# Kernel optimization log

Measured on AMD Instinct MI355X. Metric: run time of the kernel, lower is better.

Reference implementation:

```python
import jax, jax.numpy as jnp
import numpy as np

USER_NUM, ITEM_NUM = 50000, 25000
N_U, N_I = 4096, 4096
N_E, N_PRED = 262144, 65536
D, K, N_LAYERS = 64, 1000, 3
SSL_TEMP, SSL_REG, ALPHA, PROTO_REG = 0.1, 1e-6, 1.0, 8e-8


def setup_inputs() -> dict:
    key = jax.random.key(0)
    ks = jax.random.split(key, 16)
    return {
        "emb_user": jax.random.normal(ks[0], (USER_NUM, D), jnp.float32),
        "emb_item": jax.random.normal(ks[1], (ITEM_NUM, D), jnp.float32),
        "user_centroids": jax.random.normal(ks[2], (K, D), jnp.float32),
        "item_centroids": jax.random.normal(ks[3], (K, D), jnp.float32),
        "edge_u": jax.random.randint(ks[4], (N_E,), 0, N_U, jnp.int32),
        "edge_v": jax.random.randint(ks[5], (N_E,), 0, N_I, jnp.int32),
        "pos_u": jax.random.randint(ks[6], (N_PRED,), 0, N_U, jnp.int32),
        "pos_v": jax.random.randint(ks[7], (N_PRED,), 0, N_I, jnp.int32),
        "neg_u": jax.random.randint(ks[8], (N_PRED,), 0, N_U, jnp.int32),
        "neg_v": jax.random.randint(ks[9], (N_PRED,), 0, N_I, jnp.int32),
        "idx_user": jax.random.randint(ks[10], (N_U,), 0, USER_NUM, jnp.int32),
        "idx_item": jax.random.randint(ks[11], (N_I,), 0, ITEM_NUM, jnp.int32),
        "user2cluster": jax.random.randint(ks[12], (USER_NUM,), 0, K, jnp.int32),
        "item2cluster": jax.random.randint(ks[13], (ITEM_NUM,), 0, K, jnp.int32),
    }


def _l2norm(x, eps=1e-12):  # F.normalize(p=2, dim=1)
    return x / jnp.maximum(jnp.linalg.norm(x, axis=1, keepdims=True), eps)


def _ssl_loss(cur, prev, prev_total):
    nc, npv, nt = _l2norm(cur), _l2norm(prev), _l2norm(prev_total)
    pos = jnp.exp(jnp.sum(nc * npv, axis=1) / SSL_TEMP)            # [B]
    tot = jnp.exp(nc @ nt.T / SSL_TEMP).sum(axis=1)                 # [B]
    return -jnp.log(pos / tot).sum()


def _proto_loss(emb, idx, node2cluster, centroids):
    ne = _l2norm(emb)
    cents = _l2norm(centroids)                                      # run_kmeans normalizes centroids
    my_cent = cents[node2cluster[idx]]                              # [B, D]
    pos = jnp.exp(jnp.sum(ne * my_cent, axis=1) / SSL_TEMP)
    tot = jnp.exp(ne @ cents.T / SSL_TEMP).sum(axis=1)
    return -jnp.log(pos / tot).sum()


def reference(emb_user, emb_item, user_centroids, item_centroids,
              edge_u, edge_v, pos_u, pos_v, neg_u, neg_v,
              idx_user, idx_item, user2cluster, item2cluster):
    # --- symmetric-normalized bipartite GraphConv (norm='both', no weight/bias) ---
    ones_e = jnp.ones((N_E,), jnp.float32)
    deg_u = jax.ops.segment_sum(ones_e, edge_u, num_segments=N_U)
    deg_i = jax.ops.segment_sum(ones_e, edge_v, num_segments=N_I)
    inv_u = (1.0 / jnp.sqrt(jnp.maximum(deg_u, 1.0)))[:, None]      # [N_U,1]
    inv_i = (1.0 / jnp.sqrt(jnp.maximum(deg_i, 1.0)))[:, None]      # [N_I,1]

    e_u = emb_user[idx_user]                                        # initial subgraph embeddings
    e_i = emb_item[idx_item]
    res_u, res_i = e_u, e_i
    h_u, h_i = e_u, e_i
    for _ in range(N_LAYERS):
        m_u = (h_u * inv_u)[edge_u]                                 # messages along rate edges
        m_i = (h_i * inv_i)[edge_v]                                 # messages along rated-by edges
        new_i = jax.ops.segment_sum(m_u, edge_v, num_segments=N_I) * inv_i
        new_u = jax.ops.segment_sum(m_i, edge_u, num_segments=N_U) * inv_u
        h_u, h_i = new_u, new_i
        res_u = res_u + h_u
        res_i = res_i + h_i

    # --- structural-neighbour SSL loss (last layer output vs layer-0 embeddings) ---
    ssl_u = _ssl_loss(h_u, e_u, emb_user)
    ssl_i = _ssl_loss(h_i, e_i, emb_item)
    ssl_loss = SSL_REG * (ssl_u + ALPHA * ssl_i)

    # --- protoNCE loss (raw embedding-table rows vs kmeans centroids) ---
    proto_loss = PROTO_REG * (
        _proto_loss(emb_user[idx_user], idx_user, user2cluster, user_centroids)
        + _proto_loss(emb_item[idx_item], idx_item, item2cluster, item_centroids)
    )

    res_u = res_u / (N_LAYERS + 1)
    res_i = res_i / (N_LAYERS + 1)

    # --- HeteroDotProductPredictor: u_dot_v on 'rate' edges -> [E,1] ---
    pos_score = jnp.sum(res_u[pos_u] * res_i[pos_v], axis=1, keepdims=True)
    neg_score = jnp.sum(res_u[neg_u] * res_i[neg_v], axis=1, keepdims=True)
    return pos_score, neg_score, ssl_loss, proto_loss
```

## Files before the change

kernel.cpp:

```cpp
#include <hip/hip_runtime.h>
#include <hip/hip_bf16.h>

#define NU 4096
#define NI 4096
#define NE 262144
#define NPRED 65536
#define DD 64
#define KCL 1000
#define UNUM 50000
#define INUM 25000
#define INUM_PAD 25008
#define KCL_PAD 1008

typedef short sh8 __attribute__((ext_vector_type(8)));
typedef float f4 __attribute__((ext_vector_type(4)));

__device__ __forceinline__ float wred64(float x){
#pragma unroll
  for(int m=1;m<64;m<<=1) x += __shfl_xor(x,m);
  return x;
}

__device__ __forceinline__ float fast_exp2(float x){
  return __builtin_amdgcn_exp2f(x);
}

__global__ void k_hist(const int* __restrict__ eu, const int* __restrict__ ev,
                       int* cu, int* ci){
  int t = blockIdx.x*256 + threadIdx.x;
  if(t < NE){ atomicAdd(&cu[eu[t]],1); atomicAdd(&ci[ev[t]],1); }
}

__global__ void k_scan(const int* cnt_u, int* rp_u, int* cur_u, float* inv_u,
                       const int* cnt_i, int* rp_i, int* cur_i, float* inv_i){
  const int* cnt = blockIdx.x ? cnt_i : cnt_u;
  int* rp  = blockIdx.x ? rp_i  : rp_u;
  int* cur = blockIdx.x ? cur_i : cur_u;
  float* inv = blockIdx.x ? inv_i : inv_u;
  __shared__ int sdata[1024];
  int tid = threadIdx.x;
  int v[4]; int s = 0;
#pragma unroll
  for(int k=0;k<4;k++){ v[k]=cnt[tid*4+k]; s+=v[k]; }
  sdata[tid]=s; __syncthreads();
  for(int off=1; off<1024; off<<=1){
    int add = (tid>=off)? sdata[tid-off] : 0;
    __syncthreads();
    if(tid>=off) sdata[tid] += add;
    __syncthreads();
  }
  int run = sdata[tid]-s;
#pragma unroll
  for(int k=0;k<4;k++){
    int idx = tid*4+k;
    rp[idx]=run; cur[idx]=run;
    inv[idx] = 1.0f/sqrtf(fmaxf((float)v[k],1.0f));
    run += v[k];
  }
  if(tid==1023) rp[4096]=run;
}

__global__ void k_fill(const int* __restrict__ eu, const int* __restrict__ ev,
                       int* cur_u, int* cur_i, int* adj_u, int* adj_i){
  int t = blockIdx.x*256 + threadIdx.x;
  if(t < NE){
    int u=eu[t], v=ev[t];
    adj_u[atomicAdd(&cur_u[u],1)] = v;
    adj_i[atomicAdd(&cur_i[v],1)] = u;
  }
}

__global__ void k_gather(const float* __restrict__ emb_u, const float* __restrict__ emb_i,
                         const int* __restrict__ idx_u, const int* __restrict__ idx_i,
                         const float* __restrict__ inv_u, const float* __restrict__ inv_i,
                         float* e_u, float* e_i, float* res_u, float* res_i,
                         float* hs_u, float* hs_i){
  int t = blockIdx.x*256 + threadIdx.x;
  const int half = NU*DD;
  if(t < half){
    int r=t>>6;
    float v = emb_u[idx_u[r]*DD + (t&63)];
    e_u[t]=v; res_u[t]=v; hs_u[t]=v*inv_u[r];
  } else {
    int s=t-half; int r=s>>6;
    float v = emb_i[idx_i[r]*DD + (s&63)];
    e_i[s]=v; res_i[s]=v; hs_i[s]=v*inv_i[r];
  }
}

__global__ void k_conv(const int* __restrict__ rp_i, const int* __restrict__ adj_i,
                       const float* __restrict__ hsu_in, const float* __restrict__ inv_i,
                       float* h_i, float* res_i, float* hsi_out,
                       const int* __restrict__ rp_u, const int* __restrict__ adj_u,
                       const float* __restrict__ hsi_in, const float* __restrict__ inv_u,
                       float* h_u, float* res_u, float* hsu_out){
  int b = blockIdx.x, lane = threadIdx.x;
  const int* rp; const int* adj; const float* srcv; const float* inv;
  float *h, *res, *hso; int node;
  if(b < NI){ rp=rp_i; adj=adj_i; srcv=hsu_in; inv=inv_i; h=h_i; res=res_i; hso=hsi_out; node=b; }
  else      { node=b-NI; rp=rp_u; adj=adj_u; srcv=hsi_in; inv=inv_u; h=h_u; res=res_u; hso=hsu_out; }
  int s=rp[node], e=rp[node+1];
  float acc=0.f;
  for(int base=s; base<e; base+=64){
    int m = e-base;
    int myidx = adj[base + min(lane, m-1)];
    int kk = min(64, m);
    int k=0;
    for(; k+8<=kk; k+=8){
      int i0=__shfl(myidx,k  ), i1=__shfl(myidx,k+1),
          i2=__shfl(myidx,k+2), i3=__shfl(myidx,k+3),
          i4=__shfl(myidx,k+4), i5=__shfl(myidx,k+5),
          i6=__shfl(myidx,k+6), i7=__shfl(myidx,k+7);
      float v0=srcv[i0*DD+lane], v1=srcv[i1*DD+lane],
            v2=srcv[i2*DD+lane], v3=srcv[i3*DD+lane],
            v4=srcv[i4*DD+lane], v5=srcv[i5*DD+lane],
            v6=srcv[i6*DD+lane], v7=srcv[i7*DD+lane];
      acc += ((v0+v1)+(v2+v3)) + ((v4+v5)+(v6+v7));
    }
    for(; k<kk; k++) acc += srcv[__shfl(myidx,k)*DD+lane];
  }
  float iv = inv[node];
  float outv = acc*iv;
  h[node*DD+lane] = outv;
  res[node*DD+lane] += outv;
  hso[node*DD+lane] = outv*iv;
}

#define SB0 12500
#define SB1 (SB0+6252)
#define SB2 (SB1+252)
#define SB3 (SB2+252)
#define SB4 (SB3+1024)
#define SB5 (SB4+1024)
#define SB6 (SB5+1024)
#define SB7 (SB6+1024)

__global__ void k_normall(const float* __restrict__ emb_u, const float* __restrict__ emb_i,
                          const float* __restrict__ ucent, const float* __restrict__ icent,
                          const float* __restrict__ h_u, const float* __restrict__ h_i,
                          const float* __restrict__ e_u, const float* __restrict__ e_i,
                          __hip_bfloat16* ntb_u, __hip_bfloat16* ntb_i,
                          __hip_bfloat16* ncb_u, __hip_bfloat16* ncb_i,
                          __hip_bfloat16* nc_u, __hip_bfloat16* nc_i,
                          __hip_bfloat16* npv_u, __hip_bfloat16* npv_i){
  const float SC = 14.426950408889634f;
  int b = blockIdx.x;
  const float* in; __hip_bfloat16* outp; int rows; float scale; int base;
  if(b < SB0)      { in=emb_u; outp=ntb_u; rows=UNUM; scale=1.f;  base=0; }
  else if(b < SB1) { in=emb_i; outp=ntb_i; rows=INUM; scale=1.f;  base=SB0; }
  else if(b < SB2) { in=ucent; outp=ncb_u; rows=KCL;  scale=1.f;  base=SB1; }
  else if(b < SB3) { in=icent; outp=ncb_i; rows=KCL;  scale=1.f;  base=SB2; }
  else if(b < SB4) { in=h_u;   outp=nc_u;  rows=NU;   scale=SC;   base=SB3; }
  else if(b < SB5) { in=h_i;   outp=nc_i;  rows=NI;   scale=SC;   base=SB4; }
  else if(b < SB6) { in=e_u;   outp=npv_u; rows=NU;   scale=SC;   base=SB5; }
  else             { in=e_i;   outp=npv_i; rows=NI;   scale=SC;   base=SB6; }
  int row = (b-base)*4 + (threadIdx.x>>6);
  int lane = threadIdx.x & 63;
  if(row >= rows){
    outp[row*DD + lane] = __float2bfloat16(0.f);
    return;
  }
  float v = in[row*DD + lane];
  float s = wred64(v*v);
  float sc = scale / fmaxf(sqrtf(s), 1e-12f);
  outp[row*DD + lane] = __float2bfloat16(v*sc);
}

__global__ void k_pos(const float* __restrict__ h_u, const float* __restrict__ h_i,
                      const float* __restrict__ e_u, const float* __restrict__ e_i,
                      const float* __restrict__ cent_u, const float* __restrict__ cent_i,
                      const int* __restrict__ idx_u, const int* __restrict__ idx_i,
                      const int* __restrict__ u2c, const int* __restrict__ i2c,
                      float* pos4){
  int w = blockIdx.x*4 + (threadIdx.x>>6);
  int lane = threadIdx.x & 63;
  if(w >= NU) return;
  float hu=h_u[w*DD+lane], eu=e_u[w*DD+lane];
  float hi=h_i[w*DD+lane], ei=e_i[w*DD+lane];
  int cu = u2c[idx_u[w]], ci = i2c[idx_i[w]];
  float cuv = cent_u[cu*DD+lane], civ = cent_i[ci*DD+lane];
  float hh = wred64(hu*hu), ee = wred64(eu*eu), he = wred64(hu*eu);
  float h2 = wred64(hi*hi), e2 = wred64(ei*ei), hei= wred64(hi*ei);
  float ccu= wred64(cuv*cuv), ecu = wred64(eu*cuv);
  float cci= wred64(civ*civ), eci = wred64(ei*civ);
  if(lane==0){
    const float eps=1e-12f;
    pos4[0*NU+w] = he  / (fmaxf(sqrtf(hh),eps)*fmaxf(sqrtf(ee),eps));
    pos4[1*NU+w] = hei / (fmaxf(sqrtf(h2),eps)*fmaxf(sqrtf(e2),eps));
    pos4[2*NU+w] = ecu / (fmaxf(sqrtf(ee),eps)*fmaxf(sqrtf(ccu),eps));
    pos4[3*NU+w] = eci / (fmaxf(sqrtf(e2),eps)*fmaxf(sqrtf(cci),eps));
  }
}

struct EArg {
  const __hip_bfloat16* A; const __hip_bfloat16* B; float* tot;
  int nBpad; int jchunk; int ny;
};

__global__ __launch_bounds__(256,4)
void k_expsum(EArg e0, EArg e1, EArg e2, EArg e3){
  EArg e = (blockIdx.z==0)? e0 : (blockIdx.z==1)? e1 : (blockIdx.z==2)? e2 : e3;
  int bid = blockIdx.x;
  int g = bid >> 6, r6 = bid & 63;
  int y = 8*g + (r6 & 7);
  int x = r6 >> 3;
  if(y >= e.ny) return;
  int wave = threadIdx.x >> 6;
  int lane = threadIdx.x & 63;
  int row0 = (x*4 + wave)*128;
  int j_begin = y*e.jchunk;
  int j_end = min(j_begin + e.jchunk, e.nBpad);
  int r = lane & 15, kq = (lane>>4)*8;

  sh8 a0[8], a1[8];
#pragma unroll
  for(int t=0;t<8;t++){
    const short* ap = (const short*)(e.A + (row0 + t*16 + r)*DD);
    a0[t] = *(const sh8*)(ap + kq);
    a1[t] = *(const sh8*)(ap + kq + 32);
  }
  float acc[8][4];
#pragma unroll
  for(int t=0;t<8;t++)
#pragma unroll
    for(int q=0;q<4;q++) acc[t][q]=0.f;

  const short* bbase = (const short*)e.B;
  const short* bp0 = bbase + (j_begin + r)*DD + kq;
  sh8 b0 = *(const sh8*)(bp0);
  sh8 b1 = *(const sh8*)(bp0 + 32);

#pragma unroll 2
  for(int j0=j_begin; j0<j_end; j0+=16){
    const short* np = bbase + (j0 + 16 + r)*DD + kq;
    sh8 n0 = *(const sh8*)(np);
    sh8 n1 = *(const sh8*)(np + 32);
#pragma unroll
    for(int t=0;t<8;t++){
      f4 c = {0.f,0.f,0.f,0.f};
      c = __builtin_amdgcn_mfma_f32_16x16x32_bf16(a0[t], b0, c, 0,0,0);
      c = __builtin_amdgcn_mfma_f32_16x16x32_bf16(a1[t], b1, c, 0,0,0);
#pragma unroll
      for(int q=0;q<4;q++) acc[t][q] += fast_exp2(c[q]);
    }
    b0 = n0; b1 = n1;
  }
#pragma unroll
  for(int t=0;t<8;t++){
#pragma unroll
    for(int q=0;q<4;q++){
      float v = acc[t][q];
      v += __shfl_xor(v,1); v += __shfl_xor(v,2);
      v += __shfl_xor(v,4); v += __shfl_xor(v,8);
      if(r==0) atomicAdd(&e.tot[row0 + t*16 + (lane>>4)*4 + q], v);
    }
  }
}

__global__ void k_score(const float* __restrict__ res_u, const float* __restrict__ res_i,
                        const int* __restrict__ pu, const int* __restrict__ pv,
                        const int* __restrict__ nu, const int* __restrict__ nv,
                        float* out){
  int t = blockIdx.x*256 + threadIdx.x;
  int pair = t >> 4;
  int sl = t & 15;
  if(pair >= 2*NPRED) return;
  int a,b;
  if(pair < NPRED){ a=pu[pair]; b=pv[pair]; }
  else { a=nu[pair-NPRED]; b=nv[pair-NPRED]; }
  f4 xu = *(const f4*)(res_u + a*DD + sl*4);
  f4 xv = *(const f4*)(res_i + b*DD + sl*4);
  float x = xu[0]*xv[0] + xu[1]*xv[1] + xu[2]*xv[2] + xu[3]*xv[3];
  x += __shfl_xor(x,1); x += __shfl_xor(x,2);
  x += __shfl_xor(x,4); x += __shfl_xor(x,8);
  if(sl==0) out[pair] = x*(1.0f/16.0f);
}

__global__ void k_loss(const float* __restrict__ tot4, const float* __restrict__ pos4,
                       float* out){
  const float PI_ = (float)(INUM_PAD-INUM), PK_ = (float)(KCL_PAD-KCL);
  float s0=0,s1=0,s2=0,s3=0;
  for(int b=threadIdx.x; b<NU; b+=256){
    s0 += logf(tot4[0*NU+b])       - 10.f*pos4[0*NU+b];
    s1 += logf(tot4[1*NU+b] - PI_) - 10.f*pos4[1*NU+b];
    s2 += logf(tot4[2*NU+b] - PK_) - 10.f*pos4[2*NU+b];
    s3 += logf(tot4[3*NU+b] - PK_) - 10.f*pos4[3*NU+b];
  }
  s0=wred64(s0); s1=wred64(s1); s2=wred64(s2); s3=wred64(s3);
  __shared__ float ls[4][4];
  int lane=threadIdx.x&63, w=threadIdx.x>>6;
  if(lane==0){ ls[w][0]=s0; ls[w][1]=s1; ls[w][2]=s2; ls[w][3]=s3; }
  __syncthreads();
  if(threadIdx.x==0){
    float a=0,b2=0,c=0,d=0;
#pragma unroll
    for(int k=0;k<4;k++){ a+=ls[k][0]; b2+=ls[k][1]; c+=ls[k][2]; d+=ls[k][3]; }
    out[2*NPRED]   = 1e-6f*(a+b2);
    out[2*NPRED+1] = 8e-8f*(c+d);
  }
}

extern "C" void kernel_launch(void* const* d_in, const int* in_sizes, int n_in,
                              void* d_out, int out_size, void* d_ws, size_t ws_size,
                              hipStream_t stream) {
  const float* emb_user = (const float*)d_in[0];
  const float* emb_item = (const float*)d_in[1];
  const float* ucent    = (const float*)d_in[2];
  const float* icent    = (const float*)d_in[3];
  const int* edge_u = (const int*)d_in[4];
  const int* edge_v = (const int*)d_in[5];
  const int* pos_u  = (const int*)d_in[6];
  const int* pos_v  = (const int*)d_in[7];
  const int* neg_u  = (const int*)d_in[8];
  const int* neg_v  = (const int*)d_in[9];
  const int* idx_u  = (const int*)d_in[10];
  const int* idx_i  = (const int*)d_in[11];
  const int* u2c    = (const int*)d_in[12];
  const int* i2c    = (const int*)d_in[13];
  float* out = (float*)d_out;

  char* w = (char*)d_ws;
  auto alloc = [&](size_t bytes)->void*{
    void* p = (void*)w;
    w += (bytes + 255) & ~(size_t)255;
    return p;
  };
  int* cnt_u = (int*)alloc(NU*4);
  int* cnt_i = (int*)alloc(NI*4);
  int* rp_u  = (int*)alloc((NU+1)*4);
  int* rp_i  = (int*)alloc((NI+1)*4);
  int* cur_u = (int*)alloc(NU*4);
  int* cur_i = (int*)alloc(NI*4);
  int* adj_u = (int*)alloc((size_t)NE*4);
  int* adj_i = (int*)alloc((size_t)NE*4);
  float* inv_u = (float*)alloc(NU*4);
  float* inv_i = (float*)alloc(NI*4);
  float* e_u  = (float*)alloc((size_t)NU*DD*4);
  float* e_i  = (float*)alloc((size_t)NI*DD*4);
  float* h_u  = (float*)alloc((size_t)NU*DD*4);
  float* h_i  = (float*)alloc((size_t)NI*DD*4);
  float* hsA_u = (float*)alloc((size_t)NU*DD*4);
  float* hsA_i = (float*)alloc((size_t)NI*DD*4);
  float* hsB_u = (float*)alloc((size_t)NU*DD*4);
  float* hsB_i = (float*)alloc((size_t)NI*DD*4);
  float* res_u= (float*)alloc((size_t)NU*DD*4);
  float* res_i= (float*)alloc((size_t)NI*DD*4);
  __hip_bfloat16* ntb_user = (__hip_bfloat16*)alloc((size_t)(UNUM+48)*DD*2);
  __hip_bfloat16* ntb_item = (__hip_bfloat16*)alloc((size_t)(INUM_PAD+48)*DD*2);
  __hip_bfloat16* ncb_u = (__hip_bfloat16*)alloc((size_t)(KCL_PAD+48)*DD*2);
  __hip_bfloat16* ncb_i = (__hip_bfloat16*)alloc((size_t)(KCL_PAD+48)*DD*2);
  __hip_bfloat16* nc_u  = (__hip_bfloat16*)alloc((size_t)NU*DD*2);
  __hip_bfloat16* nc_i  = (__hip_bfloat16*)alloc((size_t)NI*DD*2);
  __hip_bfloat16* npv_u = (__hip_bfloat16*)alloc((size_t)NU*DD*2);
  __hip_bfloat16* npv_i = (__hip_bfloat16*)alloc((size_t)NI*DD*2);
  float* tot4 = (float*)alloc(4*NU*4);
  float* pos4 = (float*)alloc(4*NU*4);

  hipMemsetAsync(cnt_u, 0, NU*4, stream);
  hipMemsetAsync(cnt_i, 0, NI*4, stream);
  hipMemsetAsync(tot4, 0, 4*NU*4, stream);

  k_hist<<<NE/256, 256, 0, stream>>>(edge_u, edge_v, cnt_u, cnt_i);
  k_scan<<<2, 1024, 0, stream>>>(cnt_u, rp_u, cur_u, inv_u, cnt_i, rp_i, cur_i, inv_i);
  k_fill<<<NE/256, 256, 0, stream>>>(edge_u, edge_v, cur_u, cur_i, adj_u, adj_i);
  k_gather<<<2*NU*DD/256, 256, 0, stream>>>(emb_user, emb_item, idx_u, idx_i,
                                            inv_u, inv_i,
                                            e_u, e_i, res_u, res_i, hsA_u, hsA_i);
  k_conv<<<NU+NI, 64, 0, stream>>>(rp_i, adj_i, hsA_u, inv_i, h_i, res_i, hsB_i,
                                   rp_u, adj_u, hsA_i, inv_u, h_u, res_u, hsB_u);
  k_conv<<<NU+NI, 64, 0, stream>>>(rp_i, adj_i, hsB_u, inv_i, h_i, res_i, hsA_i,
                                   rp_u, adj_u, hsB_i, inv_u, h_u, res_u, hsA_u);
  k_conv<<<NU+NI, 64, 0, stream>>>(rp_i, adj_i, hsA_u, inv_i, h_i, res_i, hsB_i,
                                   rp_u, adj_u, hsA_i, inv_u, h_u, res_u, hsB_u);

  k_normall<<<SB7, 256, 0, stream>>>(emb_user, emb_item, ucent, icent,
                                     h_u, h_i, e_u, e_i,
                                     ntb_user, ntb_item, ncb_u, ncb_i,
                                     nc_u, nc_i, npv_u, npv_i);

  k_pos<<<NU/4, 256, 0, stream>>>(h_u, h_i, e_u, e_i, ucent, icent,
                                  idx_u, idx_i, u2c, i2c, pos4);

  EArg eu_ = { nc_u,  ntb_user, tot4 + 0*NU, UNUM,     1024, 49 };
  EArg ei_ = { nc_i,  ntb_item, tot4 + 1*NU, INUM_PAD, 1024, 25 };
  EArg ep0 = { npv_u, ncb_u,    tot4 + 2*NU, KCL_PAD,  48,   21 };
  EArg ep1 = { npv_i, ncb_i,    tot4 + 3*NU, KCL_PAD,  48,   21 };
  k_expsum<<<dim3(448,1,4), 256, 0, stream>>>(eu_, ei_, ep0, ep1);

  k_score<<<(2*NPRED*16)/256, 256, 0, stream>>>(res_u, res_i, pos_u, pos_v, neg_u, neg_v, out);
  k_loss<<<1, 256, 0, stream>>>(tot4, pos4, out);
}
```

Before: 239.1 us.

## Rebalance expsum work into uniform chunks with persistent grid; pack conv waves per block

The exp-sum GEMM kernel now uses a flat work list of fixed 256-column chunks across all four segments, processed by a persistent 1024-block grid with a grid-stride loop. This replaces the old 3D grid with uneven per-segment chunk sizes and many early-exit blocks, aiming for better load balance across CUs. The conv kernel packs four node-waves into each 256-thread block instead of one wave per block, which cuts block scheduling overhead. Smaller chunks mean more atomicAdds per output row and more reloads of the A fragments.

```diff
diff --git a/kernel.cpp b/kernel.cpp
--- a/kernel.cpp
+++ b/kernel.cpp
@@ -94,7 +94,8 @@
                        const int* __restrict__ rp_u, const int* __restrict__ adj_u,
                        const float* __restrict__ hsi_in, const float* __restrict__ inv_u,
                        float* h_u, float* res_u, float* hsu_out){
-  int b = blockIdx.x, lane = threadIdx.x;
+  int b = blockIdx.x*4 + (threadIdx.x>>6);
+  int lane = threadIdx.x & 63;
   const int* rp; const int* adj; const float* srcv; const float* inv;
   float *h, *res, *hso; int node;
   if(b < NI){ rp=rp_i; adj=adj_i; srcv=hsu_in; inv=inv_i; h=h_i; res=res_i; hso=hsi_out; node=b; }
@@ -192,67 +193,73 @@
   }
 }
 
-struct EArg {
-  const __hip_bfloat16* A; const __hip_bfloat16* B; float* tot;
-  int nBpad; int jchunk; int ny;
-};
+#define ECH 256
+#define EU0 1568
+#define EU1 (EU0+784)
+#define EU2 (EU1+32)
+#define EU3 (EU2+32)
+
+struct ESeg { const __hip_bfloat16* A; const __hip_bfloat16* B; float* tot; int nB; };
 
 __global__ __launch_bounds__(256,4)
-void k_expsum(EArg e0, EArg e1, EArg e2, EArg e3){
-  EArg e = (blockIdx.z==0)? e0 : (blockIdx.z==1)? e1 : (blockIdx.z==2)? e2 : e3;
-  int bid = blockIdx.x;
-  int g = bid >> 6, r6 = bid & 63;
-  int y = 8*g + (r6 & 7);
-  int x = r6 >> 3;
-  if(y >= e.ny) return;
+void k_expsum(ESeg s0, ESeg s1, ESeg s2, ESeg s3){
   int wave = threadIdx.x >> 6;
   int lane = threadIdx.x & 63;
-  int row0 = (x*4 + wave)*128;
-  int j_begin = y*e.jchunk;
-  int j_end = min(j_begin + e.jchunk, e.nBpad);
   int r = lane & 15, kq = (lane>>4)*8;
 
-  sh8 a0[8], a1[8];
-#pragma unroll
-  for(int t=0;t<8;t++){
-    const short* ap = (const short*)(e.A + (row0 + t*16 + r)*DD);
-    a0[t] = *(const sh8*)(ap + kq);
-    a1[t] = *(const sh8*)(ap + kq + 32);
-  }
-  float acc[8][4];
-#pragma unroll
-  for(int t=0;t<8;t++)
-#pragma unroll
-    for(int q=0;q<4;q++) acc[t][q]=0.f;
-
-  const short* bbase = (const short*)e.B;
-  const short* bp0 = bbase + (j_begin + r)*DD + kq;
-  sh8 b0 = *(const sh8*)(bp0);
-  sh8 b1 = *(const sh8*)(bp0 + 32);
+  for(int u = blockIdx.x; u < EU3; u += 1024){
+    ESeg s; int rem;
+    if(u < EU0)      { s = s0; rem = u; }
+    else if(u < EU1) { s = s1; rem = u-EU0; }
+    else if(u < EU2) { s = s2; rem = u-EU1; }
+    else             { s = s3; rem = u-EU2; }
+    int yc = rem >> 3, x = rem & 7;
+    int row0 = (x*4 + wave)*128;
+    int j_begin = yc*ECH;
+    int j_end = min(j_begin + ECH, s.nB);
+
+    sh8 a0[8], a1[8];
+#pragma unroll
+    for(int t=0;t<8;t++){
+      const short* ap = (const short*)(s.A + (row0 + t*16 + r)*DD);
+      a0[t] = *(const sh8*)(ap + kq);
+      a1[t] = *(const sh8*)(ap + kq + 32);
+    }
+    float acc[8][4];
+#pragma unroll
+    for(int t=0;t<8;t++)
+#pragma unroll
+      for(int q=0;q<4;q++) acc[t][q]=0.f;
+
+    const short* bbase = (const short*)s.B;
+    const short* bp0 = bbase + (j_begin + r)*DD + kq;
+    sh8 b0 = *(const sh8*)(bp0);
+    sh8 b1 = *(const sh8*)(bp0 + 32);
 
 #pragma unroll 2
-  for(int j0=j_begin; j0<j_end; j0+=16){
-    const short* np = bbase + (j0 + 16 + r)*DD + kq;
-    sh8 n0 = *(const sh8*)(np);
-    sh8 n1 = *(const sh8*)(np + 32);
+    for(int j0=j_begin; j0<j_end; j0+=16){
+      const short* np = bbase + (j0 + 16 + r)*DD + kq;
+      sh8 n0 = *(const sh8*)(np);
+      sh8 n1 = *(const sh8*)(np + 32);
+#pragma unroll
+      for(int t=0;t<8;t++){
+        f4 c = {0.f,0.f,0.f,0.f};
+        c = __builtin_amdgcn_mfma_f32_16x16x32_bf16(a0[t], b0, c, 0,0,0);
+        c = __builtin_amdgcn_mfma_f32_16x16x32_bf16(a1[t], b1, c, 0,0,0);
+#pragma unroll
+        for(int q=0;q<4;q++) acc[t][q] += fast_exp2(c[q]);
+      }
+      b0 = n0; b1 = n1;
+    }
 #pragma unroll
     for(int t=0;t<8;t++){
-      f4 c = {0.f,0.f,0.f,0.f};
-      c = __builtin_amdgcn_mfma_f32_16x16x32_bf16(a0[t], b0, c, 0,0,0);
-      c = __builtin_amdgcn_mfma_f32_16x16x32_bf16(a1[t], b1, c, 0,0,0);
-#pragma unroll
-      for(int q=0;q<4;q++) acc[t][q] += fast_exp2(c[q]);
-    }
-    b0 = n0; b1 = n1;
-  }
-#pragma unroll
-  for(int t=0;t<8;t++){
-#pragma unroll
-    for(int q=0;q<4;q++){
-      float v = acc[t][q];
-      v += __shfl_xor(v,1); v += __shfl_xor(v,2);
-      v += __shfl_xor(v,4); v += __shfl_xor(v,8);
-      if(r==0) atomicAdd(&e.tot[row0 + t*16 + (lane>>4)*4 + q], v);
+#pragma unroll
+      for(int q=0;q<4;q++){
+        float v = acc[t][q];
+        v += __shfl_xor(v,1); v += __shfl_xor(v,2);
+        v += __shfl_xor(v,4); v += __shfl_xor(v,8);
+        if(r==0) atomicAdd(&s.tot[row0 + t*16 + (lane>>4)*4 + q], v);
+      }
     }
   }
 }
@@ -366,12 +373,12 @@
   k_gather<<<2*NU*DD/256, 256, 0, stream>>>(emb_user, emb_item, idx_u, idx_i,
                                             inv_u, inv_i,
                                             e_u, e_i, res_u, res_i, hsA_u, hsA_i);
-  k_conv<<<NU+NI, 64, 0, stream>>>(rp_i, adj_i, hsA_u, inv_i, h_i, res_i, hsB_i,
-                                   rp_u, adj_u, hsA_i, inv_u, h_u, res_u, hsB_u);
-  k_conv<<<NU+NI, 64, 0, stream>>>(rp_i, adj_i, hsB_u, inv_i, h_i, res_i, hsA_i,
-                                   rp_u, adj_u, hsB_i, inv_u, h_u, res_u, hsA_u);
-  k_conv<<<NU+NI, 64, 0, stream>>>(rp_i, adj_i, hsA_u, inv_i, h_i, res_i, hsB_i,
-                                   rp_u, adj_u, hsA_i, inv_u, h_u, res_u, hsB_u);
+  k_conv<<<(NU+NI)/4, 256, 0, stream>>>(rp_i, adj_i, hsA_u, inv_i, h_i, res_i, hsB_i,
+                                        rp_u, adj_u, hsA_i, inv_u, h_u, res_u, hsB_u);
+  k_conv<<<(NU+NI)/4, 256, 0, stream>>>(rp_i, adj_i, hsB_u, inv_i, h_i, res_i, hsA_i,
+                                        rp_u, adj_u, hsB_i, inv_u, h_u, res_u, hsA_u);
+  k_conv<<<(NU+NI)/4, 256, 0, stream>>>(rp_i, adj_i, hsA_u, inv_i, h_i, res_i, hsB_i,
+                                        rp_u, adj_u, hsA_i, inv_u, h_u, res_u, hsB_u);
 
   k_normall<<<SB7, 256, 0, stream>>>(emb_user, emb_item, ucent, icent,
                                      h_u, h_i, e_u, e_i,
@@ -381,11 +388,11 @@
   k_pos<<<NU/4, 256, 0, stream>>>(h_u, h_i, e_u, e_i, ucent, icent,
                                   idx_u, idx_i, u2c, i2c, pos4);
 
-  EArg eu_ = { nc_u,  ntb_user, tot4 + 0*NU, UNUM,     1024, 49 };
-  EArg ei_ = { nc_i,  ntb_item, tot4 + 1*NU, INUM_PAD, 1024, 25 };
-  EArg ep0 = { npv_u, ncb_u,    tot4 + 2*NU, KCL_PAD,  48,   21 };
-  EArg ep1 = { npv_i, ncb_i,    tot4 + 3*NU, KCL_PAD,  48,   21 };
-  k_expsum<<<dim3(448,1,4), 256, 0, stream>>>(eu_, ei_, ep0, ep1);
+  ESeg su = { nc_u,  ntb_user, tot4 + 0*NU, UNUM };
+  ESeg si = { nc_i,  ntb_item, tot4 + 1*NU, INUM_PAD };
+  ESeg sp0= { npv_u, ncb_u,    tot4 + 2*NU, KCL_PAD };
+  ESeg sp1= { npv_i, ncb_i,    tot4 + 3*NU, KCL_PAD };
+  k_expsum<<<1024, 256, 0, stream>>>(su, si, sp0, sp1);
 
   k_score<<<(2*NPRED*16)/256, 256, 0, stream>>>(res_u, res_i, pos_u, pos_v, neg_u, neg_v, out);
   k_loss<<<1, 256, 0, stream>>>(tot4, pos4, out);
```

Measured after the change: 241.2 us. No clear change (+0.9%).
